# Kernel tuning notes

Hardware: AMD Instinct MI355X
Metric: run time of the kernel (lower is better)

## Reference

```python
import jax, jax.numpy as jnp
import numpy as np

N, T, V, C = 64, 64, 64, 64   # batch, time(=ref_channels), joints(=kpt_channels), in_channels
RED, OUT = 2, 64              # red_channels, out_channels


def setup_inputs() -> dict:
    key = jax.random.key(0)
    ks = jax.random.split(key, 8)
    s_m = (2.0 / C) ** 0.5          # kaiming-ish scale for 1x1 convs
    s_rm = (2.0 / (RED * T)) ** 0.5
    s_f = (1.0 / C) ** 0.5
    return {
        "x": jax.random.normal(ks[0], (N, T, V, C), dtype=jnp.float32),
        "A": jax.random.normal(ks[1], (T, V, V), dtype=jnp.float32) * 0.1,
        "w_m1": jax.random.normal(ks[2], (RED, C), dtype=jnp.float32) * s_m,
        "b_m1": jnp.zeros((RED,), dtype=jnp.float32),
        "w_m2": jax.random.normal(ks[3], (RED, C), dtype=jnp.float32) * s_m,
        "b_m2": jnp.zeros((RED,), dtype=jnp.float32),
        "w_rm": jax.random.normal(ks[4], (T, RED * T), dtype=jnp.float32) * s_rm,
        "b_rm": jnp.zeros((T,), dtype=jnp.float32),
        "w_f": jax.random.normal(ks[5], (OUT, C), dtype=jnp.float32) * s_f,
        "b_f": jnp.zeros((OUT,), dtype=jnp.float32),
        "alpha_m": 1,
    }


def reference(x, A, w_m1, b_m1, w_m2, b_m2, w_rm, b_rm, w_f, b_f, alpha_m):
    n = x.shape[0]
    # conv_f: pointwise Linear over channels -> (N,T,V,OUT)
    xf = jnp.einsum('ntvc,oc->ntvo', x, w_f) + b_f
    # conv_m1/conv_m2: 1x1 Conv2d over channel dim -> (N,RED,T,V)
    xm1 = jnp.einsum('ntvc,rc->nrtv', x, w_m1) + b_m1[None, :, None, None]
    xm2 = jnp.einsum('ntvc,rc->nrtv', x, w_m2) + b_m2[None, :, None, None]
    xm1 = xm1.reshape(n, RED * T, V)
    xm2 = xm2.reshape(n, RED * T, V)
    # pairwise outer difference + tanh -> (N, RED*T, V, V)
    xm = jnp.tanh(xm1[..., :, None] - xm2[..., None, :])
    # conv_rm: 1x1 conv reducing RED*T -> T channels, then scale + static adjacency
    adj = jnp.einsum('nkij,tk->ntij', xm, w_rm) + b_rm[None, :, None, None]
    adj = adj * alpha_m + A[None]          # (N,T,V,V)
    # batched matmul: dynamic adjacency x features
    out = jnp.einsum('ntij,ntjo->ntio', adj, xf)  # (N,T,V,OUT)
    return out
```

## Files before the change

kernel.cpp:

```cpp
#include <hip/hip_runtime.h>
#include <hip/hip_bf16.h>


typedef float  f32x4  __attribute__((ext_vector_type(4)));
typedef short  bf16x8 __attribute__((ext_vector_type(8)));
typedef short  bf16x4 __attribute__((ext_vector_type(4)));

static __device__ __forceinline__ short f2bf(float f) {
    __hip_bfloat16 h = __float2bfloat16(f);
    return *reinterpret_cast<short*>(&h);
}

static __device__ __forceinline__ float bf2f(short s) {
    return __uint_as_float(((unsigned)(unsigned short)s) << 16);
}

static __device__ __forceinline__ bf16x8 cvt8f(const float4 a, const float4 b) {
    bf16x8 r;
    r[0] = f2bf(a.x); r[1] = f2bf(a.y); r[2] = f2bf(a.z); r[3] = f2bf(a.w);
    r[4] = f2bf(b.x); r[5] = f2bf(b.y); r[6] = f2bf(b.z); r[7] = f2bf(b.w);
    return r;
}

static __device__ __forceinline__ bf16x8 cvt8(const float* p) {
    return cvt8f(*(const float4*)p, *(const float4*)(p + 4));
}

static __device__ __forceinline__ float tanh_fast(float x) {
    float e = __expf(2.0f * x);
    return 1.0f - 2.0f * __builtin_amdgcn_rcpf(e + 1.0f);
}

static __device__ __forceinline__ float dot4(float4 a, float4 b) {
    return a.x * b.x + a.y * b.y + a.z * b.z + a.w * b.w;
}

static __device__ __forceinline__ float alpha_decode(const int* p) {
    int raw = p[0];
    unsigned ur = (unsigned)(raw < 0 ? -raw : raw);
    return (ur < (1u << 23)) ? (float)raw : __int_as_float(raw);
}

#define MFMA16(a, b, c) __builtin_amdgcn_mfma_f32_16x16x32_bf16((a), (b), (c), 0, 0, 0)

__global__ __launch_bounds__(256) void k0_stream(
    const float* __restrict__ x,
    const float* __restrict__ w_m1, const float* __restrict__ b_m1,
    const float* __restrict__ w_m2, const float* __restrict__ b_m2,
    short* __restrict__ xbf, float* __restrict__ m1g, float* __restrict__ m2g)
{
    const int g  = blockIdx.x * 256 + threadIdx.x;
    const int R  = g >> 3;
    const int l8 = g & 7;
    const int c0 = l8 * 8;
    const int n  = R >> 12, tt = (R >> 6) & 63, v = R & 63;

    const float* xp = x + ((size_t)R << 6) + c0;
    const float4 a0 = *(const float4*)xp;
    const float4 a1 = *(const float4*)(xp + 4);

    float s0 = dot4(a0, *(const float4*)(w_m1 + c0))
             + dot4(a1, *(const float4*)(w_m1 + c0 + 4));
    float s1 = dot4(a0, *(const float4*)(w_m1 + 64 + c0))
             + dot4(a1, *(const float4*)(w_m1 + 64 + c0 + 4));
    float s2 = dot4(a0, *(const float4*)(w_m2 + c0))
             + dot4(a1, *(const float4*)(w_m2 + c0 + 4));
    float s3 = dot4(a0, *(const float4*)(w_m2 + 64 + c0))
             + dot4(a1, *(const float4*)(w_m2 + 64 + c0 + 4));

    *(bf16x8*)(xbf + ((size_t)R << 6) + c0) = cvt8f(a0, a1);

#pragma unroll
    for (int m = 1; m < 8; m <<= 1) {
        s0 += __shfl_xor(s0, m);
        s1 += __shfl_xor(s1, m);
        s2 += __shfl_xor(s2, m);
        s3 += __shfl_xor(s3, m);
    }
    if (l8 < 4) {
        float s    = (l8 == 0) ? s0 : (l8 == 1) ? s1 : (l8 == 2) ? s2 : s3;
        float bias = (l8 < 2) ? b_m1[l8] : b_m2[l8 - 2];
        float* base = (l8 < 2) ? m1g : m2g;
        base[n * 8192 + ((l8 & 1) * 64 + tt) * 64 + v] = s + bias;
    }
}

__global__ __launch_bounds__(256) void k0b_T(
    const float* __restrict__ m1g, const float* __restrict__ m2g,
    float* __restrict__ m1T, float* __restrict__ m2T)
{
    const int idx   = blockIdx.x * 256 + threadIdx.x;
    const int which = idx >> 17;
    const int r     = idx & 131071;
    const int n     = r >> 11;
    const int rr    = r & 2047;
    const int v     = rr >> 5;
    const int k0    = (rr & 31) * 4;

    const float* s = (which ? m2g : m1g) + n * 8192 + v;
    float4 o;
    o.x = s[(k0 + 0) * 64];
    o.y = s[(k0 + 1) * 64];
    o.z = s[(k0 + 2) * 64];
    o.w = s[(k0 + 3) * 64];
    float* d = (which ? m2T : m1T) + n * 8192 + v * 128 + k0;
    *(float4*)d = o;
}

__global__ __launch_bounds__(512) void k1_adj(
    const float* __restrict__ w_rm,
    const float* __restrict__ m1T,  const float* __restrict__ m2T,
    const int* __restrict__ alpha_p,
    short* __restrict__ adjm)
{
    __shared__ float m2s[64 * 132];
    __shared__ short wrs[64 * 132];

    const int b   = blockIdx.x;
    const int n   = b >> 3;
    const int i0  = (b & 7) * 8;
    const int tid = threadIdx.x;

    const float alpha = alpha_decode(alpha_p);

    {
        const float4* src = (const float4*)(m2T + n * 8192);
        for (int it = tid; it < 2048; it += 512) {
            int j = it >> 5, q = it & 31;
            *(float4*)(m2s + j * 132 + q * 4) = src[it];
        }
    }
    {
        const float4* src = (const float4*)w_rm;
        for (int it = tid; it < 2048; it += 512) {
            int t = it >> 5, q = it & 31;
            float4 v = src[it];
            bf16x4 pv;
            pv[0] = f2bf(alpha * v.x);
            pv[1] = f2bf(alpha * v.y);
            pv[2] = f2bf(alpha * v.z);
            pv[3] = f2bf(alpha * v.w);
            *(bf16x4*)(wrs + t * 132 + q * 4) = pv;
        }
    }
    __syncthreads();

    const int l = tid & 63, w = tid >> 6;
    const int lr = l & 15, lg = l >> 4;
    const int ig = i0 + w;

    float4 m1r[8];
#pragma unroll
    for (int kt = 0; kt < 4; ++kt) {
        const float* p = m1T + n * 8192 + ig * 128 + kt * 32 + lg * 8;
        m1r[kt * 2 + 0] = *(const float4*)p;
        m1r[kt * 2 + 1] = *(const float4*)(p + 4);
    }

    short* adjb = adjm + ((size_t)n << 18) + (ig << 6);

#pragma unroll 1
    for (int jt = 0; jt < 4; ++jt) {
        const float* m2row = m2s + (jt * 16 + lr) * 132;
        bf16x8 bfr[4];
#pragma unroll
        for (int kt = 0; kt < 4; ++kt) {
            const int k0 = kt * 32 + lg * 8;
            float4 b0 = *(const float4*)(m2row + k0);
            float4 b1 = *(const float4*)(m2row + k0 + 4);
            float4 a0 = m1r[kt * 2], a1 = m1r[kt * 2 + 1];
            bfr[kt][0] = f2bf(tanh_fast(a0.x - b0.x));
            bfr[kt][1] = f2bf(tanh_fast(a0.y - b0.y));
            bfr[kt][2] = f2bf(tanh_fast(a0.z - b0.z));
            bfr[kt][3] = f2bf(tanh_fast(a0.w - b0.w));
            bfr[kt][4] = f2bf(tanh_fast(a1.x - b1.x));
            bfr[kt][5] = f2bf(tanh_fast(a1.y - b1.y));
            bfr[kt][6] = f2bf(tanh_fast(a1.z - b1.z));
            bfr[kt][7] = f2bf(tanh_fast(a1.w - b1.w));
        }

        const int j0 = jt * 16 + lg * 4;
#pragma unroll
        for (int q = 0; q < 4; ++q) {
            const int tq = q * 16 + lr;
            bf16x8 af[4];
#pragma unroll
            for (int kt = 0; kt < 4; ++kt)
                af[kt] = *(const bf16x8*)(wrs + tq * 132 + kt * 32 + lg * 8);
            f32x4 acc = (f32x4){0.f, 0.f, 0.f, 0.f};
#pragma unroll
            for (int kt = 0; kt < 4; ++kt)
                acc = MFMA16(bfr[kt], af[kt], acc);
            bf16x4 pv;
            pv[0] = f2bf(acc[0]);
            pv[1] = f2bf(acc[1]);
            pv[2] = f2bf(acc[2]);
            pv[3] = f2bf(acc[3]);
            *(bf16x4*)(adjb + ((size_t)tq << 12) + j0) = pv;
        }
    }
}

__global__ __launch_bounds__(256) void k2_out(
    const short* __restrict__ adjm, const short* __restrict__ xbf,
    const float* __restrict__ Ast,  const float* __restrict__ b_rm,
    const int* __restrict__ alpha_p,
    const float* __restrict__ w_f,  const float* __restrict__ b_f,
    float* __restrict__ out)
{
    __shared__ short adjs[64 * 72];
    __shared__ short xT[64 * 72 + 32];
    __shared__ short P[64 * 104];

    const int pair = blockIdx.x;
    const int t    = pair & 63;
    const int tid  = threadIdx.x;
    const int l = tid & 63, w = tid >> 6;
    const int lr = l & 15, lg = l >> 4;

    const short* Ab = adjm + ((size_t)pair << 12);
    const short* Xb = xbf  + ((size_t)pair << 12);
    const float* At = Ast  + ((size_t)t << 12);
    float*       Ob = out  + ((size_t)pair << 12);

    const float ab = alpha_decode(alpha_p) * b_rm[t];

#pragma unroll
    for (int pass = 0; pass < 2; ++pass) {
        const int it  = pass * 256 + tid;
        const int row = it >> 3;
        const int c8  = (it & 7) * 8;
        bf16x8 s  = *(const bf16x8*)(Ab + row * 64 + c8);
        float4 a0 = *(const float4*)(At + row * 64 + c8);
        float4 a1 = *(const float4*)(At + row * 64 + c8 + 4);
        bf16x8 r;
        r[0] = f2bf(bf2f(s[0]) + a0.x + ab);
        r[1] = f2bf(bf2f(s[1]) + a0.y + ab);
        r[2] = f2bf(bf2f(s[2]) + a0.z + ab);
        r[3] = f2bf(bf2f(s[3]) + a0.w + ab);
        r[4] = f2bf(bf2f(s[4]) + a1.x + ab);
        r[5] = f2bf(bf2f(s[5]) + a1.y + ab);
        r[6] = f2bf(bf2f(s[6]) + a1.z + ab);
        r[7] = f2bf(bf2f(s[7]) + a1.w + ab);
        *(bf16x8*)(adjs + row * 72 + c8) = r;
    }

    {
        const int j  = tid >> 2;
        const int c0 = (tid & 3) * 16;
        bf16x8 r0 = *(const bf16x8*)(Xb + j * 64 + c0);
        bf16x8 r1 = *(const bf16x8*)(Xb + j * 64 + c0 + 8);
        const int g0 = (c0 >> 4) * 8;
#pragma unroll
        for (int d = 0; d < 8; ++d) {
            xT[(c0 + d) * 72 + g0 + j]     = r0[d];
            xT[(c0 + 8 + d) * 72 + g0 + j] = r1[d];
        }
    }
    if (tid < 128) {
        int row = tid >> 1, cz = 80 + (tid & 1) * 8;
        bf16x8 z = {0, 0, 0, 0, 0, 0, 0, 0};
        *(bf16x8*)(P + row * 104 + cz) = z;
    }
    __syncthreads();

    bf16x8 adjA[4][2];
#pragma unroll
    for (int mt = 0; mt < 4; ++mt)
#pragma unroll
        for (int ks = 0; ks < 2; ++ks)
            adjA[mt][ks] = *(const bf16x8*)(adjs + (mt * 16 + lr) * 72
                                            + ks * 32 + lg * 8);

    {
        bf16x8 bx[2];
#pragma unroll
        for (int ks = 0; ks < 2; ++ks)
            bx[ks] = *(const bf16x8*)(xT + (w * 16 + lr) * 72 + w * 8
                                      + ks * 32 + lg * 8);

        f32x4 acc[4];
#pragma unroll
        for (int mt = 0; mt < 4; ++mt) acc[mt] = (f32x4){0.f, 0.f, 0.f, 0.f};
#pragma unroll
        for (int ks = 0; ks < 2; ++ks)
#pragma unroll
            for (int mt = 0; mt < 4; ++mt)
                acc[mt] = MFMA16(adjA[mt][ks], bx[ks], acc[mt]);

#pragma unroll
        for (int mt = 0; mt < 4; ++mt)
#pragma unroll
            for (int e = 0; e < 4; ++e)
                P[(mt * 16 + lg * 4 + e) * 104 + w * 16 + lr] = f2bf(acc[mt][e]);

        if (w == 0) {
            bf16x8 ones = {0, 0, 0, 0, 0, 0, 0, 0};
            if (lr == 0) {
#pragma unroll
                for (int d = 0; d < 8; ++d) ones[d] = (short)0x3F80;
            }
            f32x4 accO[4];
#pragma unroll
            for (int mt = 0; mt < 4; ++mt) accO[mt] = (f32x4){0.f, 0.f, 0.f, 0.f};
#pragma unroll
            for (int ks = 0; ks < 2; ++ks)
#pragma unroll
                for (int mt = 0; mt < 4; ++mt)
                    accO[mt] = MFMA16(adjA[mt][ks], ones, accO[mt]);
#pragma unroll
            for (int mt = 0; mt < 4; ++mt)
#pragma unroll
                for (int e = 0; e < 4; ++e)
                    P[(mt * 16 + lg * 4 + e) * 104 + 64 + lr] = f2bf(accO[mt][e]);
        }
    }
    __syncthreads();

    {
        const int o = w * 16 + lr;
        bf16x8 afw[3];
#pragma unroll
        for (int ks = 0; ks < 2; ++ks)
            afw[ks] = cvt8(w_f + o * 64 + ks * 32 + lg * 8);
        {
            bf16x8 ab2 = {0, 0, 0, 0, 0, 0, 0, 0};
            if (lg == 0) ab2[0] = f2bf(b_f[o]);
            afw[2] = ab2;
        }

#pragma unroll
        for (int nt = 0; nt < 4; ++nt) {
            const int i = nt * 16 + lr;
            bf16x8 bP[3];
#pragma unroll
            for (int ks = 0; ks < 3; ++ks)
                bP[ks] = *(const bf16x8*)(P + i * 104 + ks * 32 + lg * 8);
            f32x4 acc = (f32x4){0.f, 0.f, 0.f, 0.f};
#pragma unroll
            for (int ks = 0; ks < 3; ++ks)
                acc = MFMA16(afw[ks], bP[ks], acc);
            *(f32x4*)(Ob + i * 64 + w * 16 + lg * 4) = acc;
        }
    }
}

extern "C" void kernel_launch(void* const* d_in, const int* in_sizes, int n_in,
                              void* d_out, int out_size, void* d_ws, size_t ws_size,
                              hipStream_t stream)
{
    const float* x    = (const float*)d_in[0];
    const float* A    = (const float*)d_in[1];
    const float* w_m1 = (const float*)d_in[2];
    const float* b_m1 = (const float*)d_in[3];
    const float* w_m2 = (const float*)d_in[4];
    const float* b_m2 = (const float*)d_in[5];
    const float* w_rm = (const float*)d_in[6];
    const float* b_rm = (const float*)d_in[7];
    const float* w_f  = (const float*)d_in[8];
    const float* b_f  = (const float*)d_in[9];
    const int*   alpha = (const int*)d_in[10];

    char* ws = (char*)d_ws;
    float* m1g = (float*)(ws);
    float* m2g = (float*)(ws + (size_t)2 * 1024 * 1024);
    short* adjm = (short*)(ws);
    short* xbf = (short*)(ws + (size_t)34 * 1024 * 1024);
    float* m1T = (float*)(ws + (size_t)66 * 1024 * 1024);
    float* m2T = (float*)(ws + (size_t)68 * 1024 * 1024);
    float* out = (float*)d_out;

    k0_stream<<<dim3(8192), dim3(256), 0, stream>>>(x, w_m1, b_m1, w_m2, b_m2,
                                                    xbf, m1g, m2g);
    k0b_T<<<dim3(1024), dim3(256), 0, stream>>>(m1g, m2g, m1T, m2T);
    k1_adj<<<dim3(512), dim3(512), 0, stream>>>(w_rm, m1T, m2T, alpha, adjm);
    k2_out<<<dim3(4096), dim3(256), 0, stream>>>(adjm, xbf, A, b_rm, alpha,
                                                 w_f, b_f, out);
}
```

Before: 71.21 us.

## Fuse channel-reduction and transpose kernels via shared-memory staging

Merges the x streaming/projection kernel and the separate transpose kernel into one kernel. Each block covers one batch and eight joints across all time steps, stages the projected values in shared memory and writes the transposed m1T/m2T layout directly. This removes one launch and a global round trip through the intermediate m1g/m2g buffers. In exchange the grid drops from 8192 to 512 blocks, each running an eight-iteration loop, which may reduce memory-level parallelism for the large x read.

```diff
diff --git a/kernel.cpp b/kernel.cpp
--- a/kernel.cpp
+++ b/kernel.cpp
@@ -43,68 +43,75 @@
 
 #define MFMA16(a, b, c) __builtin_amdgcn_mfma_f32_16x16x32_bf16((a), (b), (c), 0, 0, 0)
 
-__global__ __launch_bounds__(256) void k0_stream(
+__global__ __launch_bounds__(512) void k0_stream2(
     const float* __restrict__ x,
     const float* __restrict__ w_m1, const float* __restrict__ b_m1,
     const float* __restrict__ w_m2, const float* __restrict__ b_m2,
-    short* __restrict__ xbf, float* __restrict__ m1g, float* __restrict__ m2g)
+    short* __restrict__ xbf, float* __restrict__ m1T, float* __restrict__ m2T)
 {
-    const int g  = blockIdx.x * 256 + threadIdx.x;
-    const int R  = g >> 3;
-    const int l8 = g & 7;
-    const int c0 = l8 * 8;
-    const int n  = R >> 12, tt = (R >> 6) & 63, v = R & 63;
-
-    const float* xp = x + ((size_t)R << 6) + c0;
-    const float4 a0 = *(const float4*)xp;
-    const float4 a1 = *(const float4*)(xp + 4);
-
-    float s0 = dot4(a0, *(const float4*)(w_m1 + c0))
-             + dot4(a1, *(const float4*)(w_m1 + c0 + 4));
-    float s1 = dot4(a0, *(const float4*)(w_m1 + 64 + c0))
-             + dot4(a1, *(const float4*)(w_m1 + 64 + c0 + 4));
-    float s2 = dot4(a0, *(const float4*)(w_m2 + c0))
-             + dot4(a1, *(const float4*)(w_m2 + c0 + 4));
-    float s3 = dot4(a0, *(const float4*)(w_m2 + 64 + c0))
-             + dot4(a1, *(const float4*)(w_m2 + 64 + c0 + 4));
-
-    *(bf16x8*)(xbf + ((size_t)R << 6) + c0) = cvt8f(a0, a1);
-
-#pragma unroll
-    for (int m = 1; m < 8; m <<= 1) {
-        s0 += __shfl_xor(s0, m);
-        s1 += __shfl_xor(s1, m);
-        s2 += __shfl_xor(s2, m);
-        s3 += __shfl_xor(s3, m);
-    }
-    if (l8 < 4) {
-        float s    = (l8 == 0) ? s0 : (l8 == 1) ? s1 : (l8 == 2) ? s2 : s3;
-        float bias = (l8 < 2) ? b_m1[l8] : b_m2[l8 - 2];
-        float* base = (l8 < 2) ? m1g : m2g;
-        base[n * 8192 + ((l8 & 1) * 64 + tt) * 64 + v] = s + bias;
-    }
-}
-
-__global__ __launch_bounds__(256) void k0b_T(
-    const float* __restrict__ m1g, const float* __restrict__ m2g,
-    float* __restrict__ m1T, float* __restrict__ m2T)
-{
-    const int idx   = blockIdx.x * 256 + threadIdx.x;
-    const int which = idx >> 17;
-    const int r     = idx & 131071;
-    const int n     = r >> 11;
-    const int rr    = r & 2047;
-    const int v     = rr >> 5;
-    const int k0    = (rr & 31) * 4;
-
-    const float* s = (which ? m2g : m1g) + n * 8192 + v;
-    float4 o;
-    o.x = s[(k0 + 0) * 64];
-    o.y = s[(k0 + 1) * 64];
-    o.z = s[(k0 + 2) * 64];
-    o.w = s[(k0 + 3) * 64];
-    float* d = (which ? m2T : m1T) + n * 8192 + v * 128 + k0;
-    *(float4*)d = o;
+    __shared__ float msT[4][8][68];
+
+    const int b   = blockIdx.x;
+    const int n   = b >> 3;
+    const int v0  = (b & 7) * 8;
+    const int tid = threadIdx.x;
+    const int tl  = tid >> 6;
+    const int vv  = (tid >> 3) & 7;
+    const int cg  = tid & 7;
+    const int c0  = cg * 8;
+
+    const float4 w10 = *(const float4*)(w_m1 + c0);
+    const float4 w11 = *(const float4*)(w_m1 + c0 + 4);
+    const float4 w20 = *(const float4*)(w_m1 + 64 + c0);
+    const float4 w21 = *(const float4*)(w_m1 + 64 + c0 + 4);
+    const float4 w30 = *(const float4*)(w_m2 + c0);
+    const float4 w31 = *(const float4*)(w_m2 + c0 + 4);
+    const float4 w40 = *(const float4*)(w_m2 + 64 + c0);
+    const float4 w41 = *(const float4*)(w_m2 + 64 + c0 + 4);
+
+#pragma unroll 2
+    for (int it = 0; it < 8; ++it) {
+        const int t = it * 8 + tl;
+        const size_t R = ((size_t)(n * 64 + t)) * 64 + (v0 + vv);
+        const float* xp = x + (R << 6) + c0;
+        const float4 a0 = *(const float4*)xp;
+        const float4 a1 = *(const float4*)(xp + 4);
+
+        float s0 = dot4(a0, w10) + dot4(a1, w11);
+        float s1 = dot4(a0, w20) + dot4(a1, w21);
+        float s2 = dot4(a0, w30) + dot4(a1, w31);
+        float s3 = dot4(a0, w40) + dot4(a1, w41);
+
+        *(bf16x8*)(xbf + (R << 6) + c0) = cvt8f(a0, a1);
+
+#pragma unroll
+        for (int m = 1; m < 8; m <<= 1) {
+            s0 += __shfl_xor(s0, m);
+            s1 += __shfl_xor(s1, m);
+            s2 += __shfl_xor(s2, m);
+            s3 += __shfl_xor(s3, m);
+        }
+        if (cg < 4) {
+            float s = (cg == 0) ? s0 : (cg == 1) ? s1 : (cg == 2) ? s2 : s3;
+            msT[cg][vv][t] = s;
+        }
+    }
+    __syncthreads();
+
+    {
+        const int m   = tid >> 8;
+        const int rem = tid & 255;
+        const int vv2 = rem >> 5;
+        const int k0  = (rem & 31) * 4;
+        const int r   = k0 >> 6;
+        const int sel = m * 2 + r;
+        const int t0  = k0 & 63;
+        float4 val = *(const float4*)&msT[sel][vv2][t0];
+        const float bias = (m == 0) ? b_m1[r] : b_m2[r];
+        val.x += bias; val.y += bias; val.z += bias; val.w += bias;
+        float* dst = ((m == 0) ? m1T : m2T) + n * 8192 + (v0 + vv2) * 128 + k0;
+        *(float4*)dst = val;
+    }
 }
 
 __global__ __launch_bounds__(512) void k1_adj(
@@ -362,17 +369,14 @@
     const int*   alpha = (const int*)d_in[10];
 
     char* ws = (char*)d_ws;
-    float* m1g = (float*)(ws);
-    float* m2g = (float*)(ws + (size_t)2 * 1024 * 1024);
     short* adjm = (short*)(ws);
     short* xbf = (short*)(ws + (size_t)34 * 1024 * 1024);
     float* m1T = (float*)(ws + (size_t)66 * 1024 * 1024);
     float* m2T = (float*)(ws + (size_t)68 * 1024 * 1024);
     float* out = (float*)d_out;
 
-    k0_stream<<<dim3(8192), dim3(256), 0, stream>>>(x, w_m1, b_m1, w_m2, b_m2,
-                                                    xbf, m1g, m2g);
-    k0b_T<<<dim3(1024), dim3(256), 0, stream>>>(m1g, m2g, m1T, m2T);
+    k0_stream2<<<dim3(512), dim3(512), 0, stream>>>(x, w_m1, b_m1, w_m2, b_m2,
+                                                    xbf, m1T, m2T);
     k1_adj<<<dim3(512), dim3(512), 0, stream>>>(w_rm, m1T, m2T, alpha, adjm);
     k2_out<<<dim3(4096), dim3(256), 0, stream>>>(adjm, xbf, A, b_rm, alpha,
                                                  w_f, b_f, out);
```

Result: no change. 70.47 us (-1.0%).
